# Kernel optimization log

Hardware: AMD Instinct MI355X
Metric: run time of the kernel (lower is better)

Reference implementation:

```python
import jax, jax.numpy as jnp
import numpy as np

EMBED, HID, H = 1024, 1024, 16
D = HID // H
B, L = 4, 4096


def setup_inputs() -> dict:
    key = jax.random.key(0)
    ks = jax.random.split(key, 16)
    s = 0.02
    return {
        "emb": jax.random.normal(ks[0], (B, L, EMBED), jnp.float32),
        "Wa_w": jax.random.normal(ks[1], (HID, EMBED), jnp.float32) * s,
        "Wa_b": jnp.zeros((HID,), jnp.float32),
        "Wb_w": jax.random.normal(ks[2], (HID, EMBED), jnp.float32) * s,
        "Wb_b": jnp.zeros((HID,), jnp.float32),
        "Wo_w": jax.random.normal(ks[3], (HID, EMBED), jnp.float32) * s,
        "Wo_b": jnp.zeros((HID,), jnp.float32),
        "C_w": jax.random.normal(ks[4], (HID, HID), jnp.float32) * s,
        "C_b": jnp.zeros((HID,), jnp.float32),
        "ln_g": jnp.ones((HID,), jnp.float32),
        "ln_b": jnp.zeros((HID,), jnp.float32),
        "f1_w": jax.random.normal(ks[5], (4 * HID, HID), jnp.float32) * s,
        "f1_b": jnp.zeros((4 * HID,), jnp.float32),
        "f2_w": jax.random.normal(ks[6], (HID, 4 * HID), jnp.float32) * s,
        "f2_b": jnp.zeros((HID,), jnp.float32),
        "p_w": jax.random.normal(ks[7], (HID, HID), jnp.float32) * s,
        "p_b": jnp.zeros((HID,), jnp.float32),
        "head_weights": jnp.ones((H,), jnp.float32),
    }


def _layernorm(x, g, b, eps=1e-5):
    mu = jnp.mean(x, axis=-1, keepdims=True)
    var = jnp.mean(jnp.square(x - mu), axis=-1, keepdims=True)
    return (x - mu) * jax.lax.rsqrt(var + eps) * g + b


def _affine_combine(x, y):
    a1, b1 = x
    a2, b2 = y
    return a1 * a2, a2 * b1 + b2


def reference(emb, Wa_w, Wa_b, Wb_w, Wb_b, Wo_w, Wo_b, C_w, C_b, ln_g, ln_b,
              f1_w, f1_b, f2_w, f2_b, p_w, p_b, head_weights):
    Bv, Lv, _ = emb.shape
    a = jnp.tanh(emb @ Wa_w.T + Wa_b).reshape(Bv, Lv, H, D)
    b = (emb @ Wb_w.T + Wb_b).reshape(Bv, Lv, H, D)
    w = (emb @ Wo_w.T + Wo_b).reshape(Bv, Lv, H, D)
    # h_t = a_t * h_{t-1} + b_t, h_0 = 0 -> parallel associative scan over L
    _, h_seq = jax.lax.associative_scan(_affine_combine, (a, b), axis=1)
    # batched per-step C projection over full hidden dim
    c_out = (h_seq.reshape(Bv, Lv, HID) @ C_w.T + C_b).reshape(Bv, Lv, H, D)
    z = (head_weights[None, None, :, None] * (c_out + w)).reshape(Bv, Lv, HID)
    u = z + _layernorm(z, ln_g, ln_b)
    ffn = jax.nn.gelu(u @ f1_w.T + f1_b, approximate=False)
    out = ffn @ f2_w.T + f2_b
    return (u + out) @ p_w.T + p_b
```

## Files before the change

### kernel.cpp

```cpp
#include <hip/hip_runtime.h>
#include <hip/hip_bf16.h>

typedef __attribute__((ext_vector_type(8))) short short8;
typedef __attribute__((ext_vector_type(4))) float f32x4;

#define DEVI static __device__ __forceinline__

constexpr int HID = 1024;
constexpr int BB = 4, LL = 4096;
constexpr int MROWS = BB * LL;
constexpr int NCH = 64, TCH = 64;

constexpr size_t ELN_EMB  = 0;
constexpr size_t ELN_WABO = 16777216;
constexpr size_t ELN_CW   = 19922944;
constexpr size_t ELN_F1   = 20971520;
constexpr size_t ELN_F2   = 25165824;
constexpr size_t ELN_PW   = 29360128;
constexpr size_t ELN_END  = 30408704;
constexpr size_t POOL_BYTES = ELN_END * 2;

constexpr size_t OFF_ABW = POOL_BYTES;
constexpr size_t OFF_H   = OFF_ABW + (size_t)MROWS*3072*2;
constexpr size_t OFF_U   = OFF_H  + (size_t)MROWS*1024*2;
constexpr size_t OFF_AGG = OFF_U  + (size_t)MROWS*1024*2;
constexpr size_t AG_ELEMS = (size_t)BB * NCH * HID;
constexpr size_t WS_NEEDED = OFF_AGG + AG_ELEMS * 4 * 3;

DEVI unsigned short f2b(float x) {
  unsigned u = __float_as_uint(x);
  return (unsigned short)((u + 0x7fffu + ((u >> 16) & 1u)) >> 16);
}
DEVI float b2f(unsigned short u) { return __uint_as_float((unsigned)u << 16); }

DEVI float fast_tanh(float y) {
  y = fminf(fmaxf(y, -10.f), 10.f);
  float e = __expf(2.f * y);
  return (e - 1.f) / (e + 1.f);
}
DEVI float gelu_fast(float x) {
  float t = 0.7978845608028654f * (x + 0.044715f * x * x * x);
  return 0.5f * x * (1.f + fast_tanh(t));
}

DEVI void gload_lds16(const unsigned short* g, unsigned short* l) {
  __builtin_amdgcn_global_load_lds(
      (const __attribute__((address_space(1))) void*)g,
      (__attribute__((address_space(3))) void*)l, 16, 0, 0);
}
DEVI void sbar() { __builtin_amdgcn_s_barrier(); }

constexpr long CH_EMB = 16777216 / 8;
constexpr long CH_W   = 1048576 / 8;
constexpr long CH_F   = 4194304 / 8;
constexpr long SEG1 = CH_EMB;
constexpr long SEG2 = SEG1 + CH_W;
constexpr long SEG3 = SEG2 + CH_W;
constexpr long SEG4 = SEG3 + CH_W;
constexpr long SEG5 = SEG4 + CH_W;
constexpr long SEG6 = SEG5 + CH_F;
constexpr long SEG7 = SEG6 + CH_F;
constexpr long SEG8 = SEG7 + CH_W;

__global__ __launch_bounds__(256) void convert_all(
    const float* __restrict__ emb, const float* __restrict__ wa,
    const float* __restrict__ wb,  const float* __restrict__ wo,
    const float* __restrict__ cw,  const float* __restrict__ f1,
    const float* __restrict__ f2,  const float* __restrict__ pw,
    unsigned short* __restrict__ dst) {
  const long stride = (long)gridDim.x * blockDim.x;
  for (long ck = (long)blockIdx.x * blockDim.x + threadIdx.x; ck < SEG8; ck += stride) {
    const float* s; size_t d;
    if (ck < SEG1)      { s = emb + (size_t)ck * 8;        d = ELN_EMB + (size_t)ck * 8; }
    else if (ck < SEG2) { s = wa + (size_t)(ck-SEG1) * 8;  d = ELN_WABO + (size_t)(ck-SEG1) * 8; }
    else if (ck < SEG3) { s = wb + (size_t)(ck-SEG2) * 8;  d = ELN_WABO + 1048576 + (size_t)(ck-SEG2) * 8; }
    else if (ck < SEG4) { s = wo + (size_t)(ck-SEG3) * 8;  d = ELN_WABO + 2097152 + (size_t)(ck-SEG3) * 8; }
    else if (ck < SEG5) { s = cw + (size_t)(ck-SEG4) * 8;  d = ELN_CW + (size_t)(ck-SEG4) * 8; }
    else if (ck < SEG6) { s = f1 + (size_t)(ck-SEG5) * 8;  d = ELN_F1 + (size_t)(ck-SEG5) * 8; }
    else if (ck < SEG7) { s = f2 + (size_t)(ck-SEG6) * 8;  d = ELN_F2 + (size_t)(ck-SEG6) * 8; }
    else                { s = pw + (size_t)(ck-SEG7) * 8;  d = ELN_PW + (size_t)(ck-SEG7) * 8; }
    float4 x = *(const float4*)s;
    float4 y = *(const float4*)(s + 4);
    short8 o;
    o[0]=(short)f2b(x.x); o[1]=(short)f2b(x.y); o[2]=(short)f2b(x.z); o[3]=(short)f2b(x.w);
    o[4]=(short)f2b(y.x); o[5]=(short)f2b(y.y); o[6]=(short)f2b(y.z); o[7]=(short)f2b(y.w);
    *(short8*)(dst + d) = o;
  }
}

template <int EPI>
__global__ __launch_bounds__(512) void gemm256(
    const unsigned short* __restrict__ A, const unsigned short* __restrict__ Bw,
    int K, int NT, int ldo, int addld,
    const float* __restrict__ biasA, const float* __restrict__ biasB,
    const float* __restrict__ biasW,
    const unsigned short* __restrict__ addB, const float* __restrict__ hw,
    float* __restrict__ outF, unsigned short* __restrict__ outB) {
  __shared__ alignas(16) unsigned short lds[4][16384];
  const int tid = threadIdx.x;
  const int lane = tid & 63, wave = tid >> 6;
  const int wr = wave >> 2, wc = wave & 3;
  const int arow0 = blockIdx.x * 256, bcol0 = blockIdx.y * 256;
  f32x4 acc[8][4] = {};
  const int fm = lane & 15, fg = lane >> 4;
  const int sA = (fg ^ (fm & 7)) * 8;
  const int sB = ((4 + fg) ^ (fm & 7)) * 8;

#define MKSRC(l)                                                                   \
  const unsigned short* src##l; {                                                  \
    const int row_ = (tid >> 3) + 64 * l;                                          \
    const int c_ = (tid & 7) ^ (row_ & 7);                                         \
    src##l = (c_ < 4) ? A + (size_t)(arow0 + row_) * K + c_ * 8                    \
                      : Bw + (size_t)(bcol0 + row_) * K + (c_ - 4) * 8; }
  MKSRC(0) MKSRC(1) MKSRC(2) MKSRC(3)
#undef MKSRC

#define STAGE(p, t) do { const int ko_ = (t) * 32;                                 \
    gload_lds16(src0 + ko_, &lds[p][tid * 8]);                                     \
    gload_lds16(src1 + ko_, &lds[p][tid * 8 + 4096]);                              \
    gload_lds16(src2 + ko_, &lds[p][tid * 8 + 8192]);                              \
    gload_lds16(src3 + ko_, &lds[p][tid * 8 + 12288]); } while (0)

  STAGE(0, 0);
  if (NT > 1) STAGE(1, 1);
  if (NT > 2) STAGE(2, 2);
  asm volatile("s_waitcnt vmcnt(8)" ::: "memory");
  sbar();

  for (int t = 0; t < NT; ++t) {
    const int p = t & 3;
    const unsigned short* LA = &lds[p][(wr * 128 + fm) * 64];
    const unsigned short* LB = &lds[p][(wc * 64 + fm) * 64];
    short8 af[4], bf[4];
    if (t + 3 < NT) STAGE((t + 3) & 3, t + 3);
#pragma unroll
    for (int n = 0; n < 4; ++n) bf[n] = *(const short8*)(LB + n * 1024 + sB);
#pragma unroll
    for (int m = 0; m < 4; ++m) af[m] = *(const short8*)(LA + m * 1024 + sA);
    __builtin_amdgcn_s_setprio(1);
#pragma unroll
    for (int m = 0; m < 4; ++m)
#pragma unroll
      for (int n = 0; n < 4; ++n)
        acc[m][n] = __builtin_amdgcn_mfma_f32_16x16x32_bf16(af[m], bf[n], acc[m][n], 0, 0, 0);
    __builtin_amdgcn_s_setprio(0);
    sbar();
#pragma unroll
    for (int m = 0; m < 4; ++m) af[m] = *(const short8*)(LA + 4096 + m * 1024 + sA);
    __builtin_amdgcn_s_setprio(1);
#pragma unroll
    for (int m = 0; m < 4; ++m)
#pragma unroll
      for (int n = 0; n < 4; ++n)
        acc[4 + m][n] = __builtin_amdgcn_mfma_f32_16x16x32_bf16(af[m], bf[n], acc[4 + m][n], 0, 0, 0);
    __builtin_amdgcn_s_setprio(0);
    const int nleft = NT - 2 - t;
    if (nleft >= 2)      asm volatile("s_waitcnt vmcnt(8)" ::: "memory");
    else if (nleft == 1) asm volatile("s_waitcnt vmcnt(4)" ::: "memory");
    else                 asm volatile("s_waitcnt vmcnt(0)" ::: "memory");
    sbar();
    __builtin_amdgcn_sched_barrier(0);
  }
#undef STAGE

  const int crow = (lane >> 4) * 4, ccol = lane & 15;
#pragma unroll
  for (int m = 0; m < 8; ++m) {
    const int row0 = arow0 + wr * 128 + (m >> 2) * 64 + (m & 3) * 16 + crow;
#pragma unroll
    for (int n = 0; n < 4; ++n) {
      const int col = bcol0 + wc * 64 + n * 16 + ccol;
#pragma unroll
      for (int r = 0; r < 4; ++r) {
        const size_t orow = (size_t)(row0 + r);
        float x = acc[m][n][r];
        if constexpr (EPI == 0) {
          const int cb = col >> 10;
          const float* bp = (cb == 0) ? biasA : (cb == 1 ? biasB : biasW);
          x += bp[col & 1023];
          if (cb == 0) x = fast_tanh(x);
          outB[orow * 3072 + col] = f2b(x);
        } else if constexpr (EPI == 1) {
          x += biasA[col] + b2f(addB[orow * (size_t)addld + col]);
          x *= hw[col >> 6];
          outB[orow * (size_t)ldo + col] = f2b(x);
        } else if constexpr (EPI == 2) {
          x += biasA[col];
          outB[orow * (size_t)ldo + col] = f2b(gelu_fast(x));
        } else if constexpr (EPI == 3) {
          x += biasA[col] + b2f(addB[orow * (size_t)addld + col]);
          outB[orow * (size_t)ldo + col] = f2b(x);
        } else {
          outF[orow * (size_t)ldo + col] = x + biasA[col];
        }
      }
    }
  }
}

__global__ __launch_bounds__(256) void scan_p1(const unsigned short* __restrict__ abw,
                                               float* __restrict__ agA,
                                               float* __restrict__ agB) {
  const int idx = blockIdx.x;
  const int cg = idx & 3, ch = (idx >> 2) & (NCH - 1), bb = idx >> 8;
  const int c = cg * 256 + threadIdx.x;
  const size_t base = ((size_t)bb * LL + (size_t)ch * TCH) * 3072 + c;
  float A = 1.f, Bg = 0.f;
#pragma unroll 4
  for (int t = 0; t < TCH; ++t) {
    float at = b2f(abw[base + (size_t)t * 3072]);
    float bt = b2f(abw[base + (size_t)t * 3072 + 1024]);
    Bg = fmaf(at, Bg, bt);
    A *= at;
  }
  const size_t o = ((size_t)bb * NCH + ch) * HID + c;
  agA[o] = A;
  agB[o] = Bg;
}

__global__ __launch_bounds__(256) void scan_p2(const float* __restrict__ agA,
                                               const float* __restrict__ agB,
                                               float* __restrict__ pre) {
  const int gid = blockIdx.x * 256 + threadIdx.x;
  const int bb = gid >> 10, c = gid & 1023;
  float h = 0.f;
  for (int ch = 0; ch < NCH; ++ch) {
    const size_t o = ((size_t)bb * NCH + ch) * HID + c;
    pre[o] = h;
    h = fmaf(agA[o], h, agB[o]);
  }
}

__global__ __launch_bounds__(256) void scan_p3(const unsigned short* __restrict__ abw,
                                               const float* __restrict__ pre,
                                               unsigned short* __restrict__ hout) {
  const int idx = blockIdx.x;
  const int cg = idx & 3, ch = (idx >> 2) & (NCH - 1), bb = idx >> 8;
  const int c = cg * 256 + threadIdx.x;
  const size_t base = ((size_t)bb * LL + (size_t)ch * TCH) * 3072 + c;
  const size_t hbase = ((size_t)bb * LL + (size_t)ch * TCH) * HID + c;
  float h = pre[((size_t)bb * NCH + ch) * HID + c];
#pragma unroll 4
  for (int t = 0; t < TCH; ++t) {
    float at = b2f(abw[base + (size_t)t * 3072]);
    float bt = b2f(abw[base + (size_t)t * 3072 + 1024]);
    h = fmaf(at, h, bt);
    hout[hbase + (size_t)t * HID] = f2b(h);
  }
}

__global__ __launch_bounds__(256) void ln_kernel(const unsigned short* __restrict__ abw,
                                                 const float* __restrict__ gam,
                                                 const float* __restrict__ bet,
                                                 unsigned short* __restrict__ u) {
  const int wave = threadIdx.x >> 6, lane = threadIdx.x & 63;
  const int row = blockIdx.x * 4 + wave;
  const unsigned short* zr = abw + (size_t)row * 3072 + lane * 16;
  short8 z0 = *(const short8*)zr;
  short8 z1 = *(const short8*)(zr + 8);
  float x[16];
#pragma unroll
  for (int e = 0; e < 8; ++e) {
    x[e]     = b2f((unsigned short)z0[e]);
    x[8 + e] = b2f((unsigned short)z1[e]);
  }
  float s = 0.f, s2 = 0.f;
#pragma unroll
  for (int e = 0; e < 16; ++e) { s += x[e]; s2 += x[e] * x[e]; }
#pragma unroll
  for (int off = 32; off > 0; off >>= 1) {
    s += __shfl_xor(s, off, 64);
    s2 += __shfl_xor(s2, off, 64);
  }
  const float mu = s * (1.f / 1024.f);
  const float var = s2 * (1.f / 1024.f) - mu * mu;
  const float rs = rsqrtf(var + 1e-5f);
  const float* gp = gam + lane * 16;
  const float* bp = bet + lane * 16;
  short8 o0, o1;
#pragma unroll
  for (int e = 0; e < 8; ++e) {
    float v0 = x[e]     + (x[e]     - mu) * rs * gp[e]     + bp[e];
    float v1 = x[8 + e] + (x[8 + e] - mu) * rs * gp[8 + e] + bp[8 + e];
    o0[e] = (short)f2b(v0);
    o1[e] = (short)f2b(v1);
  }
  unsigned short* ur = u + (size_t)row * HID + lane * 16;
  *(short8*)ur = o0;
  *(short8*)(ur + 8) = o1;
}

extern "C" void kernel_launch(void* const* d_in, const int* in_sizes, int n_in,
                              void* d_out, int out_size, void* d_ws, size_t ws_size,
                              hipStream_t stream) {
  if (ws_size < WS_NEEDED) return;

  const float* emb   = (const float*)d_in[0];
  const float* Wa_w  = (const float*)d_in[1];
  const float* Wa_b  = (const float*)d_in[2];
  const float* Wb_w  = (const float*)d_in[3];
  const float* Wb_b  = (const float*)d_in[4];
  const float* Wo_w  = (const float*)d_in[5];
  const float* Wo_b  = (const float*)d_in[6];
  const float* C_w   = (const float*)d_in[7];
  const float* C_b   = (const float*)d_in[8];
  const float* ln_g  = (const float*)d_in[9];
  const float* ln_b  = (const float*)d_in[10];
  const float* f1_w  = (const float*)d_in[11];
  const float* f1_b  = (const float*)d_in[12];
  const float* f2_w  = (const float*)d_in[13];
  const float* f2_b  = (const float*)d_in[14];
  const float* p_w   = (const float*)d_in[15];
  const float* p_b   = (const float*)d_in[16];
  const float* headw = (const float*)d_in[17];

  char* ws = (char*)d_ws;
  unsigned short* bfp  = (unsigned short*)ws;
  unsigned short* abwB = (unsigned short*)(ws + OFF_ABW);
  unsigned short* hB   = (unsigned short*)(ws + OFF_H);
  unsigned short* uB   = (unsigned short*)(ws + OFF_U);
  unsigned short* ffnB = abwB;
  float* agA = (float*)(ws + OFF_AGG);
  float* agB = agA + AG_ELEMS;
  float* pre = agB + AG_ELEMS;

  convert_all<<<2048, 256, 0, stream>>>(emb, Wa_w, Wb_w, Wo_w, C_w, f1_w, f2_w, p_w, bfp);

  gemm256<0><<<dim3(64, 12), 512, 0, stream>>>(
      bfp + ELN_EMB, bfp + ELN_WABO, 1024, 32, 3072, 0,
      Wa_b, Wb_b, Wo_b, nullptr, nullptr, nullptr, abwB);

  scan_p1<<<BB * NCH * 4, 256, 0, stream>>>(abwB, agA, agB);
  scan_p2<<<16, 256, 0, stream>>>(agA, agB, pre);
  scan_p3<<<BB * NCH * 4, 256, 0, stream>>>(abwB, pre, hB);

  gemm256<1><<<dim3(64, 4), 512, 0, stream>>>(
      hB, bfp + ELN_CW, 1024, 32, 3072, 3072,
      C_b, nullptr, nullptr, abwB + 2048, headw, nullptr, abwB);

  ln_kernel<<<4096, 256, 0, stream>>>(abwB, ln_g, ln_b, uB);

  gemm256<2><<<dim3(64, 16), 512, 0, stream>>>(
      uB, bfp + ELN_F1, 1024, 32, 4096, 0,
      f1_b, nullptr, nullptr, nullptr, nullptr, nullptr, ffnB);

  gemm256<3><<<dim3(64, 4), 512, 0, stream>>>(
      ffnB, bfp + ELN_F2, 4096, 128, 1024, 1024,
      f2_b, nullptr, nullptr, uB, nullptr, nullptr, uB);

  gemm256<4><<<dim3(64, 4), 512, 0, stream>>>(
      uB, bfp + ELN_PW, 1024, 32, 1024, 0,
      p_b, nullptr, nullptr, nullptr, nullptr, (float*)d_out, nullptr);
}
```

Baseline: 581.9 us.

## Restructure GEMM main loop into 8-phase ping-pong schedule with split staging

Replaces the 4-stage ring buffer K-loop in the bf16 GEMM with a double-buffered schedule that handles two K-tiles per outer iteration. Each iteration runs eight phases, and each phase interleaves half of a tile's global-to-LDS loads with a half-tile of MFMAs. B fragments are reused across the two M halves. The goal is finer-grained overlap of memory loads with MFMA work and fewer barrier stalls per tile. In exchange, the tail iterations issue redundant wraparound loads of tiles 0 and 1, the vmcnt tracking becomes more complex, and there are more barriers per K step.

```diff
diff --git a/kernel.cpp b/kernel.cpp
--- a/kernel.cpp
+++ b/kernel.cpp
@@ -91,12 +91,12 @@
 template <int EPI>
 __global__ __launch_bounds__(512) void gemm256(
     const unsigned short* __restrict__ A, const unsigned short* __restrict__ Bw,
-    int K, int NT, int ldo, int addld,
+    int K, int NITER, int ldo, int addld,
     const float* __restrict__ biasA, const float* __restrict__ biasB,
     const float* __restrict__ biasW,
     const unsigned short* __restrict__ addB, const float* __restrict__ hw,
     float* __restrict__ outF, unsigned short* __restrict__ outB) {
-  __shared__ alignas(16) unsigned short lds[4][16384];
+  __shared__ alignas(16) unsigned short lds[2][2][16384];
   const int tid = threadIdx.x;
   const int lane = tid & 63, wave = tid >> 6;
   const int wr = wave >> 2, wc = wave & 3;
@@ -105,6 +105,7 @@
   const int fm = lane & 15, fg = lane >> 4;
   const int sA = (fg ^ (fm & 7)) * 8;
   const int sB = ((4 + fg) ^ (fm & 7)) * 8;
+  const int NT = NITER * 2;
 
 #define MKSRC(l)                                                                   \
   const unsigned short* src##l; {                                                  \
@@ -115,53 +116,58 @@
   MKSRC(0) MKSRC(1) MKSRC(2) MKSRC(3)
 #undef MKSRC
 
-#define STAGE(p, t) do { const int ko_ = (t) * 32;                                 \
-    gload_lds16(src0 + ko_, &lds[p][tid * 8]);                                     \
-    gload_lds16(src1 + ko_, &lds[p][tid * 8 + 4096]);                              \
-    gload_lds16(src2 + ko_, &lds[p][tid * 8 + 8192]);                              \
-    gload_lds16(src3 + ko_, &lds[p][tid * 8 + 12288]); } while (0)
-
-  STAGE(0, 0);
-  if (NT > 1) STAGE(1, 1);
-  if (NT > 2) STAGE(2, 2);
+#define STG0(bf, ks, kt) do { const int ko_ = (kt) * 64 + (ks) * 32;               \
+    gload_lds16(src0 + ko_, &lds[bf][ks][tid * 8]);                                \
+    gload_lds16(src1 + ko_, &lds[bf][ks][4096 + tid * 8]); } while (0)
+#define STG1(bf, ks, kt) do { const int ko_ = (kt) * 64 + (ks) * 32;               \
+    gload_lds16(src2 + ko_, &lds[bf][ks][8192 + tid * 8]);                         \
+    gload_lds16(src3 + ko_, &lds[bf][ks][12288 + tid * 8]); } while (0)
+
+  short8 bfr[4];
+#define PHASE(BUF, KS, MH, NEWB, STG, DOVM) do {                                   \
+    const unsigned short* lab = &lds[BUF][KS][0];                                  \
+    if (NEWB) {                                                                    \
+      _Pragma("unroll") for (int n = 0; n < 4; ++n)                                \
+        bfr[n] = *(const short8*)(lab + (wc * 64 + n * 16 + fm) * 64 + sB);        \
+    }                                                                              \
+    short8 af[4];                                                                  \
+    _Pragma("unroll") for (int m = 0; m < 4; ++m)                                  \
+      af[m] = *(const short8*)(lab + (wr * 128 + MH * 64 + m * 16 + fm) * 64 + sA);\
+    STG;                                                                           \
+    __builtin_amdgcn_s_setprio(1);                                                 \
+    _Pragma("unroll") for (int m = 0; m < 4; ++m)                                  \
+      _Pragma("unroll") for (int n = 0; n < 4; ++n)                                \
+        acc[MH * 4 + m][n] = __builtin_amdgcn_mfma_f32_16x16x32_bf16(              \
+            af[m], bfr[n], acc[MH * 4 + m][n], 0, 0, 0);                           \
+    __builtin_amdgcn_s_setprio(0);                                                 \
+    if (DOVM) asm volatile("s_waitcnt vmcnt(8)" ::: "memory");                     \
+    sbar();                                                                        \
+    __builtin_amdgcn_sched_barrier(0);                                             \
+  } while (0)
+
+  STG0(0, 0, 0); STG1(0, 0, 0);
+  STG0(0, 1, 0); STG1(0, 1, 0);
+  STG0(1, 0, 1); STG1(1, 0, 1);
   asm volatile("s_waitcnt vmcnt(8)" ::: "memory");
   sbar();
-
-  for (int t = 0; t < NT; ++t) {
-    const int p = t & 3;
-    const unsigned short* LA = &lds[p][(wr * 128 + fm) * 64];
-    const unsigned short* LB = &lds[p][(wc * 64 + fm) * 64];
-    short8 af[4], bf[4];
-    if (t + 3 < NT) STAGE((t + 3) & 3, t + 3);
-#pragma unroll
-    for (int n = 0; n < 4; ++n) bf[n] = *(const short8*)(LB + n * 1024 + sB);
-#pragma unroll
-    for (int m = 0; m < 4; ++m) af[m] = *(const short8*)(LA + m * 1024 + sA);
-    __builtin_amdgcn_s_setprio(1);
-#pragma unroll
-    for (int m = 0; m < 4; ++m)
-#pragma unroll
-      for (int n = 0; n < 4; ++n)
-        acc[m][n] = __builtin_amdgcn_mfma_f32_16x16x32_bf16(af[m], bf[n], acc[m][n], 0, 0, 0);
-    __builtin_amdgcn_s_setprio(0);
-    sbar();
-#pragma unroll
-    for (int m = 0; m < 4; ++m) af[m] = *(const short8*)(LA + 4096 + m * 1024 + sA);
-    __builtin_amdgcn_s_setprio(1);
-#pragma unroll
-    for (int m = 0; m < 4; ++m)
-#pragma unroll
-      for (int n = 0; n < 4; ++n)
-        acc[4 + m][n] = __builtin_amdgcn_mfma_f32_16x16x32_bf16(af[m], bf[n], acc[4 + m][n], 0, 0, 0);
-    __builtin_amdgcn_s_setprio(0);
-    const int nleft = NT - 2 - t;
-    if (nleft >= 2)      asm volatile("s_waitcnt vmcnt(8)" ::: "memory");
-    else if (nleft == 1) asm volatile("s_waitcnt vmcnt(4)" ::: "memory");
-    else                 asm volatile("s_waitcnt vmcnt(0)" ::: "memory");
-    sbar();
-    __builtin_amdgcn_sched_barrier(0);
-  }
-#undef STAGE
+  __builtin_amdgcn_sched_barrier(0);
+
+  for (int it = 0; it < NITER; ++it) {
+    const int t1 = 2 * it + 1;
+    const int t2 = (2 * it + 2 < NT) ? 2 * it + 2 : 0;
+    const int t3 = (2 * it + 3 < NT) ? 2 * it + 3 : 1;
+    PHASE(0, 0, 0, true,  STG0(1, 1, t1), false);
+    PHASE(0, 0, 1, false, STG1(1, 1, t1), true);
+    PHASE(0, 1, 0, true,  STG0(0, 0, t2), false);
+    PHASE(0, 1, 1, false, STG1(0, 0, t2), true);
+    PHASE(1, 0, 0, true,  STG0(0, 1, t2), false);
+    PHASE(1, 0, 1, false, STG1(0, 1, t2), true);
+    PHASE(1, 1, 0, true,  STG0(1, 0, t3), false);
+    PHASE(1, 1, 1, false, STG1(1, 0, t3), true);
+  }
+#undef PHASE
+#undef STG0
+#undef STG1
 
   const int crow = (lane >> 4) * 4, ccol = lane & 15;
 #pragma unroll
@@ -327,7 +333,7 @@
   convert_all<<<2048, 256, 0, stream>>>(emb, Wa_w, Wb_w, Wo_w, C_w, f1_w, f2_w, p_w, bfp);
 
   gemm256<0><<<dim3(64, 12), 512, 0, stream>>>(
-      bfp + ELN_EMB, bfp + ELN_WABO, 1024, 32, 3072, 0,
+      bfp + ELN_EMB, bfp + ELN_WABO, 1024, 8, 3072, 0,
       Wa_b, Wb_b, Wo_b, nullptr, nullptr, nullptr, abwB);
 
   scan_p1<<<BB * NCH * 4, 256, 0, stream>>>(abwB, agA, agB);
@@ -335,20 +341,20 @@
   scan_p3<<<BB * NCH * 4, 256, 0, stream>>>(abwB, pre, hB);
 
   gemm256<1><<<dim3(64, 4), 512, 0, stream>>>(
-      hB, bfp + ELN_CW, 1024, 32, 3072, 3072,
+      hB, bfp + ELN_CW, 1024, 8, 3072, 3072,
       C_b, nullptr, nullptr, abwB + 2048, headw, nullptr, abwB);
 
   ln_kernel<<<4096, 256, 0, stream>>>(abwB, ln_g, ln_b, uB);
 
   gemm256<2><<<dim3(64, 16), 512, 0, stream>>>(
-      uB, bfp + ELN_F1, 1024, 32, 4096, 0,
+      uB, bfp + ELN_F1, 1024, 8, 4096, 0,
       f1_b, nullptr, nullptr, nullptr, nullptr, nullptr, ffnB);
 
   gemm256<3><<<dim3(64, 4), 512, 0, stream>>>(
-      ffnB, bfp + ELN_F2, 4096, 128, 1024, 1024,
+      ffnB, bfp + ELN_F2, 4096, 32, 1024, 1024,
       f2_b, nullptr, nullptr, uB, nullptr, nullptr, uB);
 
   gemm256<4><<<dim3(64, 4), 512, 0, stream>>>(
-      uB, bfp + ELN_PW, 1024, 32, 1024, 0,
+      uB, bfp + ELN_PW, 1024, 8, 1024, 0,
       p_b, nullptr, nullptr, nullptr, nullptr, (float*)d_out, nullptr);
 }
```

After: 563.0 us. 1.03x faster.
